# Performance work log

Hardware: AMD Instinct MI355X
Metric: run time of the kernel (lower is better)

## Reference

```python
import jax, jax.numpy as jnp
import numpy as np

# --- architecture constants (match init_kwargs) ---
SLEN = 104
PTILE = 8
STEP = 2
N_BANDS = 2
MAX_DET = 2
N_SRC_PARAMS = 2
ENC_C = 20
ENC_HIDDEN = 256
# dim_out_all = 0.5*D*(D+1)*(4+2*n_source_params) + 1 + D  (probs over n_sources + per-count loc/flux mean+logvar)
DIM_OUT = int(0.5 * MAX_DET * (MAX_DET + 1) * (4 + 2 * N_SRC_PARAMS)) + 1 + MAX_DET  # 27


def _p(key, shape, scale=0.02):
    return scale * jax.random.normal(key, shape, dtype=jnp.float32)


def setup_inputs() -> dict:
    key = jax.random.key(0)
    ks = jax.random.split(key, 14)
    flat_in = ENC_C * PTILE * PTILE  # 20*8*8 = 1280
    return {
        "images": jax.random.normal(ks[0], (32, N_BANDS, SLEN, SLEN), dtype=jnp.float32),
        "conv1_w": _p(ks[1], (ENC_C, N_BANDS, 3, 3)),
        "conv1_b": _p(ks[2], (ENC_C,)),
        "conv2_w": _p(ks[3], (ENC_C, ENC_C, 3, 3)),
        "conv2_b": _p(ks[4], (ENC_C,)),
        "fc1_w": _p(ks[5], (ENC_HIDDEN, flat_in)),
        "fc1_b": _p(ks[6], (ENC_HIDDEN,)),
        "fc2_w": _p(ks[7], (ENC_HIDDEN, ENC_HIDDEN)),
        "fc2_b": _p(ks[8], (ENC_HIDDEN,)),
        "fc3_w": _p(ks[9], (ENC_HIDDEN, ENC_HIDDEN)),
        "fc3_b": _p(ks[10], (ENC_HIDDEN,)),
        "fcf_w": _p(ks[11], (DIM_OUT, ENC_HIDDEN)),
        "fcf_b": _p(ks[12], (DIM_OUT,)),
    }


def _tile_images(images):
    # torch tile_images: (B, C, slen, slen) -> (B * n_ptiles, C, P, P), tiles row-major over (x, y)
    B, C = images.shape[0], images.shape[1]
    patches = jax.lax.conv_general_dilated_patches(
        images, filter_shape=(PTILE, PTILE), window_strides=(STEP, STEP), padding="VALID"
    )  # (B, C*P*P, Hn, Wn) with feature dim ordered (C, P, P)
    Hn, Wn = patches.shape[2], patches.shape[3]
    p = patches.reshape(B, C, PTILE, PTILE, Hn, Wn)
    p = p.transpose(0, 4, 5, 1, 2, 3)  # (B, Hn, Wn, C, P, P)
    return p.reshape(B * Hn * Wn, C, PTILE, PTILE)


def _conv(x, w, b):
    y = jax.lax.conv_general_dilated(
        x, w, window_strides=(1, 1), padding="SAME",
        dimension_numbers=("NCHW", "OIHW", "NCHW"),
    )
    return y + b[None, :, None, None]


def reference(images, conv1_w, conv1_b, conv2_w, conv2_b,
              fc1_w, fc1_b, fc2_w, fc2_b, fc3_w, fc3_b, fcf_w, fcf_b):
    ptiles = _tile_images(images)                       # (B*nT, C, P, P)
    h = jax.nn.relu(_conv(ptiles, conv1_w, conv1_b))    # (B*nT, 20, P, P)
    h = jax.nn.relu(_conv(h, conv2_w, conv2_b))
    h = h.reshape(h.shape[0], -1)                       # Flatten -> (B*nT, 1280)
    h = jax.nn.relu(h @ fc1_w.T + fc1_b)
    h = jax.nn.relu(h @ fc2_w.T + fc2_b)
    h = jax.nn.relu(h @ fc3_w.T + fc3_b)
    return h @ fcf_w.T + fcf_b                          # (B*nT, dim_out_all)
```

## Files before the change

kernel.cpp:

```cpp
#include <hip/hip_runtime.h>
#include <hip/hip_bf16.h>

#define NPATCH 76832
#define NBLK   601
#define K1     1280

typedef __attribute__((ext_vector_type(8))) short  short8;
typedef __attribute__((ext_vector_type(4))) float  floatx4;

__device__ __forceinline__ unsigned short f2b(float f) {
    unsigned int u = __builtin_bit_cast(unsigned int, f);
    u += 0x7FFFu + ((u >> 16) & 1u);
    return (unsigned short)(u >> 16);
}
__device__ __forceinline__ unsigned int pk2(float a, float b) {
    __hip_bfloat162 h = __float22bfloat162_rn(make_float2(a, b));
    unsigned int u;
    __builtin_memcpy(&u, &h, 4);
    return u;
}

__device__ __forceinline__ void gload_lds16(const unsigned short* g, unsigned short* l) {
    __builtin_amdgcn_global_load_lds(
        (__attribute__((address_space(1))) void*)g,
        (__attribute__((address_space(3))) void*)l,
        16, 0, 0);
}

__device__ __host__ __forceinline__ int swz8(int row, int i) {
    return (((row & 1) * 4 + i) ^ ((row >> 1) & 7));
}

__global__ void prep(const float* __restrict__ f1w, const float* __restrict__ f2w,
                     const float* __restrict__ f3w, const float* __restrict__ c1w,
                     const float* __restrict__ c2w, const float* __restrict__ ffw,
                     unsigned short* __restrict__ W1F, unsigned short* __restrict__ W2F,
                     unsigned short* __restrict__ W3F, unsigned short* __restrict__ W1T,
                     unsigned short* __restrict__ W2T, unsigned short* __restrict__ WfF) {
    int i = blockIdx.x * 256 + threadIdx.x;
    if (i < 327680) {
        int o = i / 1280, k = i - o * 1280;
        int dst = ((k >> 5) * 16 + (o >> 6) * 4 + ((o >> 4) & 3)) * 512
                + (((k >> 3) & 3) * 16 + (o & 15)) * 8 + (k & 7);
        W1F[dst] = f2b(f1w[i]);
        return;
    }
    i -= 327680;
    if (i < 65536) {
        int o = i >> 8, k = i & 255;
        int dst = ((k >> 5) * 16 + (o >> 6) * 4 + ((o >> 4) & 3)) * 512
                + (((k >> 3) & 3) * 16 + (o & 15)) * 8 + (k & 7);
        W2F[dst] = f2b(f2w[i]);
        return;
    }
    i -= 65536;
    if (i < 65536) {
        int o = i >> 8, k = i & 255;
        int dst = ((k >> 5) * 16 + (o >> 6) * 4 + ((o >> 4) & 3)) * 512
                + (((k >> 3) & 3) * 16 + (o & 15)) * 8 + (k & 7);
        W3F[dst] = f2b(f3w[i]);
        return;
    }
    i -= 65536;
    if (i < 1024) {
        int o = i >> 5, k = i & 31;
        unsigned short v = 0;
        if (o < 20 && k < 18) v = f2b(c1w[o * 18 + k]);
        W1T[(o >> 1) * 64 + swz8(o, k >> 3) * 8 + (k & 7)] = v;
        return;
    }
    i -= 1024;
    if (i < 9216) {
        int tap = i >> 10, rem = i & 1023, o = rem >> 5, c = rem & 31;
        unsigned short v = 0;
        if (o < 20 && c < 20) v = f2b(c2w[o * 180 + c * 9 + tap]);
        W2T[tap * 1024 + (o >> 1) * 64 + swz8(o, c >> 3) * 8 + (c & 7)] = v;
        return;
    }
    i -= 9216;
    if (i < 8192) {
        int o = i >> 8, k = i & 255;
        unsigned short v = (o < 27) ? f2b(ffw[o * 256 + k]) : (unsigned short)0;
        int dst = ((k >> 5) * 2 + (o >> 4)) * 512
                + (((k >> 3) & 3) * 16 + (o & 15)) * 8 + (k & 7);
        WfF[dst] = v;
    }
}

__global__ __launch_bounds__(256, 3) void conv_mfma(
    const float* __restrict__ img,
    const unsigned short* __restrict__ W1T, const float* __restrict__ b1,
    const unsigned short* __restrict__ W2T, const float* __restrict__ b2,
    unsigned short* __restrict__ X, int row0)
{
    __shared__ alignas(16) unsigned short s_buf[8 * 2048 + 64];
    __shared__ alignas(16) unsigned short s_w1t[1024];
    __shared__ alignas(16) unsigned short s_w2t[9216];
    __shared__ float s_b1[32], s_b2[32];
    constexpr int ZOFF = 8 * 2048;

    const int tid = threadIdx.x;
    for (int d = tid; d < 512; d += 256)  ((unsigned int*)s_w1t)[d] = ((const unsigned int*)W1T)[d];
    for (int d = tid; d < 4608; d += 256) ((unsigned int*)s_w2t)[d] = ((const unsigned int*)W2T)[d];
    if (tid < 32) {
        ((unsigned int*)&s_buf[ZOFF])[tid] = 0u;
        s_b1[tid] = (tid < 20) ? b1[tid] : 0.f;
        s_b2[tid] = (tid < 20) ? b2[tid] : 0.f;
    }

    const int q = tid >> 5, t = tid & 31;
    const int Pl = blockIdx.x * 8 + q;
    const int Pi = row0 + Pl;
    const bool valid = Pi < NPATCH;
    int b = 0, hi = 0, wi = 0;
    if (valid) { b = Pi / 2401; int rem = Pi - b * 2401; hi = rem / 49; wi = rem - hi * 49; }
    const int py = t >> 2, px0 = (t & 3) * 2;
    const float* ib = img + (long long)b * 21632 + (hi * 2) * 104 + (wi * 2);

    float win[2][3][4];
    #pragma unroll
    for (int c = 0; c < 2; ++c)
        #pragma unroll
        for (int dy = 0; dy < 3; ++dy) {
            int ny = py + dy - 1;
            int nyc = ny < 0 ? 0 : (ny > 7 ? 7 : ny);
            #pragma unroll
            for (int dxw = 0; dxw < 4; ++dxw) {
                int nx = px0 + dxw - 1;
                int nxc = nx < 0 ? 0 : (nx > 7 ? 7 : nx);
                win[c][dy][dxw] = ib[c * 10816 + nyc * 104 + nxc];
            }
        }

    #pragma unroll
    for (int j = 0; j < 2; ++j) {
        const int px = px0 + j, pl = py * 8 + px;
        float val[18];
        #pragma unroll
        for (int c = 0; c < 2; ++c)
            #pragma unroll
            for (int dy = 0; dy < 3; ++dy) {
                int ny = py + dy - 1;
                bool rok = valid && ((unsigned)ny < 8u);
                #pragma unroll
                for (int dx = 0; dx < 3; ++dx) {
                    int nx = px + dx - 1;
                    bool ok = rok && ((unsigned)nx < 8u);
                    val[c * 9 + dy * 3 + dx] = ok ? win[c][dy][dx + j] : 0.f;
                }
            }
        alignas(16) unsigned int au[16];
        #pragma unroll
        for (int i = 0; i < 9; ++i) au[i] = pk2(val[2 * i], val[2 * i + 1]);
        #pragma unroll
        for (int i = 9; i < 16; ++i) au[i] = 0u;
        unsigned short* base = &s_buf[q * 2048 + (pl >> 1) * 64];
        #pragma unroll
        for (int i = 0; i < 4; ++i)
            *(uint4*)&base[swz8(pl, i) * 8] = ((const uint4*)au)[i];
    }
    __syncthreads();

    const int wave = tid >> 6, lane = tid & 63;
    const int l15 = lane & 15, quad = lane >> 4;
    const int p0 = wave * 2;

    int boffB[2];
    #pragma unroll
    for (int i = 0; i < 2; ++i) {
        int oo = i * 16 + l15;
        boffB[i] = (oo >> 1) * 64 + swz8(oo, quad) * 8;
    }

    short8 a1f[2];
    #pragma unroll
    for (int mt = 0; mt < 2; ++mt) a1f[mt] = *(const short8*)&s_w1t[boffB[mt]];

    floatx4 acc1[2][2][4] = {};
    #pragma unroll
    for (int pp = 0; pp < 2; ++pp)
        #pragma unroll
        for (int nt = 0; nt < 4; ++nt) {
            int pix = nt * 16 + l15;
            short8 pf = *(const short8*)&s_buf[(p0 + pp) * 2048 + (pix >> 1) * 64 + swz8(pix, quad) * 8];
            #pragma unroll
            for (int mt = 0; mt < 2; ++mt)
                acc1[pp][mt][nt] = __builtin_amdgcn_mfma_f32_16x16x32_bf16(a1f[mt], pf, acc1[pp][mt][nt], 0, 0, 0);
        }

    float bv1[2][4];
    #pragma unroll
    for (int mt = 0; mt < 2; ++mt)
        #pragma unroll
        for (int r = 0; r < 4; ++r) bv1[mt][r] = s_b1[mt * 16 + quad * 4 + r];

    #pragma unroll
    for (int pp = 0; pp < 2; ++pp)
        #pragma unroll
        for (int mt = 0; mt < 2; ++mt)
            #pragma unroll
            for (int nt = 0; nt < 4; ++nt) {
                floatx4 v = acc1[pp][mt][nt];
                uint2 w;
                w.x = pk2(fmaxf(v[0] + bv1[mt][0], 0.f), fmaxf(v[1] + bv1[mt][1], 0.f));
                w.y = pk2(fmaxf(v[2] + bv1[mt][2], 0.f), fmaxf(v[3] + bv1[mt][3], 0.f));
                int pix = nt * 16 + l15;
                int off = (p0 + pp) * 2048 + (pix >> 1) * 64
                        + swz8(pix, mt * 2 + (quad >> 1)) * 8 + (quad & 1) * 4;
                *(uint2*)&s_buf[off] = w;
            }

    int syv[4], pxv[4];
    #pragma unroll
    for (int mt = 0; mt < 4; ++mt) { int p = mt * 16 + l15; syv[mt] = p >> 3; pxv[mt] = p & 7; }

    floatx4 acc2[2][4][2] = {};
    #pragma unroll 1
    for (int dy = 0; dy < 3; ++dy) {
        int sy[4]; bool okY[4];
        #pragma unroll
        for (int mt = 0; mt < 4; ++mt) {
            sy[mt] = syv[mt] + dy - 1;
            okY[mt] = (unsigned)sy[mt] < 8u;
        }
        #pragma unroll
        for (int dx = 0; dx < 3; ++dx) {
            const int tap = dy * 3 + dx;
            short8 bf0 = *(const short8*)&s_w2t[tap * 1024 + boffB[0]];
            short8 bf1 = *(const short8*)&s_w2t[tap * 1024 + boffB[1]];
            #pragma unroll
            for (int mt = 0; mt < 4; ++mt) {
                int sx = pxv[mt] + dx - 1;
                bool ok = okY[mt] & ((unsigned)sx < 8u);
                int ps = sy[mt] * 8 + sx;
                int offl = (ps >> 1) * 64 + swz8(ps, quad) * 8;
                #pragma unroll
                for (int pp = 0; pp < 2; ++pp) {
                    int off = ok ? ((p0 + pp) * 2048 + offl) : (ZOFF + quad * 8);
                    short8 af = *(const short8*)&s_buf[off];
                    acc2[pp][mt][0] = __builtin_amdgcn_mfma_f32_16x16x32_bf16(af, bf0, acc2[pp][mt][0], 0, 0, 0);
                    acc2[pp][mt][1] = __builtin_amdgcn_mfma_f32_16x16x32_bf16(af, bf1, acc2[pp][mt][1], 0, 0, 0);
                }
            }
        }
    }

    #pragma unroll
    for (int pp = 0; pp < 2; ++pp) {
        unsigned short* xrow = X + (long long)(blockIdx.x * 8 + p0 + pp) * K1;
        #pragma unroll
        for (int nt = 0; nt < 2; ++nt) {
            const int col = nt * 16 + l15;
            if (col < 20) {
                const float bv = s_b2[col];
                #pragma unroll
                for (int mt = 0; mt < 4; ++mt) {
                    floatx4 v = acc2[pp][mt][nt];
                    uint2 w;
                    w.x = pk2(fmaxf(v[0] + bv, 0.f), fmaxf(v[1] + bv, 0.f));
                    w.y = pk2(fmaxf(v[2] + bv, 0.f), fmaxf(v[3] + bv, 0.f));
                    *(uint2*)&xrow[col * 64 + mt * 16 + quad * 4] = w;
                }
            }
        }
    }
}

__global__ __launch_bounds__(256, 3) void fc_all(
    const unsigned short* __restrict__ X,
    const unsigned short* __restrict__ W1F, const unsigned short* __restrict__ W2F,
    const unsigned short* __restrict__ W3F, const unsigned short* __restrict__ WfF,
    const float* __restrict__ b1, const float* __restrict__ b2,
    const float* __restrict__ b3, const float* __restrict__ bf_,
    float* __restrict__ out, int row0)
{
    __shared__ alignas(16) unsigned short s_mem[16384];

    const int tid = threadIdx.x;
    const int m0 = blockIdx.x * 64;
    const int wave = tid >> 6, lane = tid & 63;
    const int l15 = lane & 15, quad = lane >> 4;

    floatx4 acc[4][4];
    #pragma unroll
    for (int mt = 0; mt < 4; ++mt)
        #pragma unroll
        for (int nt = 0; nt < 4; ++nt) acc[mt][nt] = floatx4{0.f, 0.f, 0.f, 0.f};

    const unsigned short* xsrc = X + (long long)(m0 + wave * 16 + l15) * 1280 + quad * 8;
    auto stage = [&](int buf, int c) {
        unsigned short* dst = &s_mem[buf * 4096 + wave * 512];
        gload_lds16(xsrc + (2 * c) * 32, dst);
        gload_lds16(xsrc + (2 * c + 1) * 32, dst + 2048);
    };

    stage(0, 0);
    __syncthreads();
    #pragma unroll 2
    for (int c = 0; c < 20; ++c) {
        short8 af[2][4];
        #pragma unroll
        for (int kh = 0; kh < 2; ++kh)
            #pragma unroll
            for (int mt = 0; mt < 4; ++mt)
                af[kh][mt] = *(const short8*)(W1F + (((2 * c + kh) * 16) + wave * 4 + mt) * 512 + lane * 8);
        __builtin_amdgcn_sched_barrier(0);
        if (c < 19) stage((c + 1) & 1, c + 1);
        const int bb = (c & 1) * 4096;
        __builtin_amdgcn_s_setprio(1);
        #pragma unroll
        for (int kh = 0; kh < 2; ++kh) {
            short8 bf[4];
            #pragma unroll
            for (int nt = 0; nt < 4; ++nt)
                bf[nt] = *(const short8*)&s_mem[bb + (kh * 4 + nt) * 512 + lane * 8];
            #pragma unroll
            for (int mt = 0; mt < 4; ++mt)
                #pragma unroll
                for (int nt = 0; nt < 4; ++nt)
                    acc[mt][nt] = __builtin_amdgcn_mfma_f32_16x16x32_bf16(af[kh][mt], bf[nt], acc[mt][nt], 0, 0, 0);
        }
        __builtin_amdgcn_s_setprio(0);
        __syncthreads();
    }

    #pragma unroll
    for (int mt = 0; mt < 4; ++mt) {
        const int obase = wave * 64 + mt * 16 + quad * 4;
        const float v0 = b1[obase], v1 = b1[obase + 1], v2 = b1[obase + 2], v3 = b1[obase + 3];
        const int slot = (wave * 2 + (mt >> 1)) * 4;
        const int qk = (mt & 1) * 2 + (quad >> 1);
        #pragma unroll
        for (int nt = 0; nt < 4; ++nt) {
            floatx4 v = acc[mt][nt];
            uint2 w;
            w.x = pk2(fmaxf(v[0] + v0, 0.f), fmaxf(v[1] + v1, 0.f));
            w.y = pk2(fmaxf(v[2] + v2, 0.f), fmaxf(v[3] + v3, 0.f));
            *(uint2*)&s_mem[(slot + nt) * 512 + qk * 128 + l15 * 8 + (quad & 1) * 4] = w;
        }
    }
    __syncthreads();

    #pragma unroll 1
    for (int layer = 0; layer < 2; ++layer) {
        const unsigned short* Wp = (layer == 0) ? W2F : W3F;
        const float* bp = (layer == 0) ? b2 : b3;

        #pragma unroll
        for (int mt = 0; mt < 4; ++mt)
            #pragma unroll
            for (int nt = 0; nt < 4; ++nt) acc[mt][nt] = floatx4{0.f, 0.f, 0.f, 0.f};

        short8 afc[4];
        #pragma unroll
        for (int mt = 0; mt < 4; ++mt)
            afc[mt] = *(const short8*)(Wp + (wave * 4 + mt) * 512 + lane * 8);

        #pragma unroll
        for (int it = 0; it < 8; ++it) {
            short8 afn[4];
            if (it < 7) {
                #pragma unroll
                for (int mt = 0; mt < 4; ++mt)
                    afn[mt] = *(const short8*)(Wp + ((it + 1) * 16 + wave * 4 + mt) * 512 + lane * 8);
            }
            short8 bf[4];
            #pragma unroll
            for (int nt = 0; nt < 4; ++nt)
                bf[nt] = *(const short8*)&s_mem[(it * 4 + nt) * 512 + lane * 8];
            __builtin_amdgcn_s_setprio(1);
            #pragma unroll
            for (int mt = 0; mt < 4; ++mt)
                #pragma unroll
                for (int nt = 0; nt < 4; ++nt)
                    acc[mt][nt] = __builtin_amdgcn_mfma_f32_16x16x32_bf16(afc[mt], bf[nt], acc[mt][nt], 0, 0, 0);
            __builtin_amdgcn_s_setprio(0);
            if (it < 7) {
                #pragma unroll
                for (int mt = 0; mt < 4; ++mt) afc[mt] = afn[mt];
            }
        }
        __syncthreads();
        #pragma unroll
        for (int mt = 0; mt < 4; ++mt) {
            const int obase = wave * 64 + mt * 16 + quad * 4;
            const float v0 = bp[obase], v1 = bp[obase + 1], v2 = bp[obase + 2], v3 = bp[obase + 3];
            const int slot = (wave * 2 + (mt >> 1)) * 4;
            const int qk = (mt & 1) * 2 + (quad >> 1);
            #pragma unroll
            for (int nt = 0; nt < 4; ++nt) {
                floatx4 v = acc[mt][nt];
                uint2 w;
                w.x = pk2(fmaxf(v[0] + v0, 0.f), fmaxf(v[1] + v1, 0.f));
                w.y = pk2(fmaxf(v[2] + v2, 0.f), fmaxf(v[3] + v3, 0.f));
                *(uint2*)&s_mem[(slot + nt) * 512 + qk * 128 + l15 * 8 + (quad & 1) * 4] = w;
            }
        }
        __syncthreads();
    }

    floatx4 accf[2] = {floatx4{0.f, 0.f, 0.f, 0.f}, floatx4{0.f, 0.f, 0.f, 0.f}};
    const int myrow = wave * 16 + l15;
    #pragma unroll
    for (int w8 = 0; w8 < 8; ++w8) {
        short8 bfr = *(const short8*)&s_mem[(w8 * 4 + wave) * 512 + lane * 8];
        #pragma unroll
        for (int mt = 0; mt < 2; ++mt) {
            short8 afr = *(const short8*)(WfF + (w8 * 2 + mt) * 512 + lane * 8);
            accf[mt] = __builtin_amdgcn_mfma_f32_16x16x32_bf16(afr, bfr, accf[mt], 0, 0, 0);
        }
    }
    const int grow = row0 + m0 + myrow;
    if (grow < NPATCH) {
        #pragma unroll
        for (int mt = 0; mt < 2; ++mt) {
            #pragma unroll
            for (int r = 0; r < 4; ++r) {
                int o = mt * 16 + quad * 4 + r;
                if (o < 27)
                    out[(long long)grow * 27 + o] = accf[mt][r] + bf_[o];
            }
        }
    }
}

extern "C" void kernel_launch(void* const* d_in, const int* in_sizes, int n_in,
                              void* d_out, int out_size, void* d_ws, size_t ws_size,
                              hipStream_t stream) {
    const float* images = (const float*)d_in[0];
    const float* c1w = (const float*)d_in[1];
    const float* c1b = (const float*)d_in[2];
    const float* c2w = (const float*)d_in[3];
    const float* c2b = (const float*)d_in[4];
    const float* f1w = (const float*)d_in[5];
    const float* f1b = (const float*)d_in[6];
    const float* f2w = (const float*)d_in[7];
    const float* f2b_ = (const float*)d_in[8];
    const float* f3w = (const float*)d_in[9];
    const float* f3b = (const float*)d_in[10];
    const float* ffw = (const float*)d_in[11];
    const float* ffb = (const float*)d_in[12];

    const long long W1_E = 327680, W2_E = 65536, W3_E = 65536;
    const long long W1T_E = 1024, W2T_E = 9216, WF_E = 8192;
    const long long WB = (W1_E + W2_E + W3_E + W1T_E + W2T_E + WF_E) * 2;
    char* ws = (char*)d_ws;
    unsigned short* W1F = (unsigned short*)ws;
    unsigned short* W2F = W1F + W1_E;
    unsigned short* W3F = W2F + W2_E;
    unsigned short* W1T = W3F + W3_E;
    unsigned short* W2T = W1T + W1T_E;
    unsigned short* WfF = W2T + W2T_E;
    unsigned short* X   = (unsigned short*)(ws + WB);

    long long avail = (long long)ws_size - WB - 256;
    int nb_max = (int)(avail / 327680LL);
    if (nb_max < 1) nb_max = 1;
    if (nb_max > NBLK) nb_max = NBLK;
    int nchunks = (NBLK + nb_max - 1) / nb_max;
    int nb_even = (NBLK + nchunks - 1) / nchunks;

    prep<<<1864, 256, 0, stream>>>(f1w, f2w, f3w, c1w, c2w, ffw, W1F, W2F, W3F, W1T, W2T, WfF);

    for (int b0 = 0; b0 < NBLK; b0 += nb_even) {
        int nb = NBLK - b0; if (nb > nb_even) nb = nb_even;
        int row0 = b0 * 128;
        int rows = nb * 128;

        conv_mfma<<<rows / 8, 256, 0, stream>>>(images, W1T, c1b, W2T, c2b, X, row0);
        fc_all<<<rows / 64, 256, 0, stream>>>(X, W1F, W2F, W3F, WfF,
                                              f1b, f2b_, f3b, ffb, (float*)d_out, row0);
    }
}
```

Measured before the change: 293.5 us.

## Drop LDS weight staging in conv kernel and prefetch fc1 weights in registers

The conv kernel no longer copies the conv weights and biases into shared memory. Each wave loads its weight fragments and biases straight from global memory, and the block-wide barrier after patch staging is removed because each wave only reads patches its own lanes wrote. Zero padding now reads a known-zero slot inside the patch buffer instead of a separate zero region. Smaller LDS use and launch_bounds raised to 4 are meant to raise occupancy. fc_all double-buffers the fc1 weight fragments in registers so the next chunk's weights load while the current chunk's MFMAs run, at the cost of more VGPRs.

After: 605.7 us. 2.06x slower.

```diff
diff --git a/kernel.cpp b/kernel.cpp
--- a/kernel.cpp
+++ b/kernel.cpp
@@ -87,25 +87,43 @@
     }
 }
 
-__global__ __launch_bounds__(256, 3) void conv_mfma(
+__global__ __launch_bounds__(256, 4) void conv_mfma(
     const float* __restrict__ img,
     const unsigned short* __restrict__ W1T, const float* __restrict__ b1,
     const unsigned short* __restrict__ W2T, const float* __restrict__ b2,
     unsigned short* __restrict__ X, int row0)
 {
-    __shared__ alignas(16) unsigned short s_buf[8 * 2048 + 64];
-    __shared__ alignas(16) unsigned short s_w1t[1024];
-    __shared__ alignas(16) unsigned short s_w2t[9216];
-    __shared__ float s_b1[32], s_b2[32];
-    constexpr int ZOFF = 8 * 2048;
+    __shared__ alignas(16) unsigned short s_buf[8 * 2048];
 
     const int tid = threadIdx.x;
-    for (int d = tid; d < 512; d += 256)  ((unsigned int*)s_w1t)[d] = ((const unsigned int*)W1T)[d];
-    for (int d = tid; d < 4608; d += 256) ((unsigned int*)s_w2t)[d] = ((const unsigned int*)W2T)[d];
-    if (tid < 32) {
-        ((unsigned int*)&s_buf[ZOFF])[tid] = 0u;
-        s_b1[tid] = (tid < 20) ? b1[tid] : 0.f;
-        s_b2[tid] = (tid < 20) ? b2[tid] : 0.f;
+    const int wave = tid >> 6, lane = tid & 63;
+    const int l15 = lane & 15, quad = lane >> 4;
+
+    int boffB[2];
+    #pragma unroll
+    for (int i = 0; i < 2; ++i) {
+        int oo = i * 16 + l15;
+        boffB[i] = (oo >> 1) * 64 + swz8(oo, quad) * 8;
+    }
+
+    short8 a1f[2];
+    #pragma unroll
+    for (int mt = 0; mt < 2; ++mt) a1f[mt] = *(const short8*)(W1T + boffB[mt]);
+    float bv1[2][4];
+    #pragma unroll
+    for (int mt = 0; mt < 2; ++mt)
+        #pragma unroll
+        for (int r = 0; r < 4; ++r) {
+            int idx = mt * 16 + quad * 4 + r;
+            float v = b1[idx < 20 ? idx : 19];
+            bv1[mt][r] = (idx < 20) ? v : 0.f;
+        }
+    float bv2[2];
+    #pragma unroll
+    for (int nt = 0; nt < 2; ++nt) {
+        int col = nt * 16 + l15;
+        float v = b2[col < 20 ? col : 19];
+        bv2[nt] = (col < 20) ? v : 0.f;
     }
 
     const int q = tid >> 5, t = tid & 31;
@@ -159,22 +177,8 @@
         for (int i = 0; i < 4; ++i)
             *(uint4*)&base[swz8(pl, i) * 8] = ((const uint4*)au)[i];
     }
-    __syncthreads();
-
-    const int wave = tid >> 6, lane = tid & 63;
-    const int l15 = lane & 15, quad = lane >> 4;
+
     const int p0 = wave * 2;
-
-    int boffB[2];
-    #pragma unroll
-    for (int i = 0; i < 2; ++i) {
-        int oo = i * 16 + l15;
-        boffB[i] = (oo >> 1) * 64 + swz8(oo, quad) * 8;
-    }
-
-    short8 a1f[2];
-    #pragma unroll
-    for (int mt = 0; mt < 2; ++mt) a1f[mt] = *(const short8*)&s_w1t[boffB[mt]];
 
     floatx4 acc1[2][2][4] = {};
     #pragma unroll
@@ -187,12 +191,6 @@
             for (int mt = 0; mt < 2; ++mt)
                 acc1[pp][mt][nt] = __builtin_amdgcn_mfma_f32_16x16x32_bf16(a1f[mt], pf, acc1[pp][mt][nt], 0, 0, 0);
         }
-
-    float bv1[2][4];
-    #pragma unroll
-    for (int mt = 0; mt < 2; ++mt)
-        #pragma unroll
-        for (int r = 0; r < 4; ++r) bv1[mt][r] = s_b1[mt * 16 + quad * 4 + r];
 
     #pragma unroll
     for (int pp = 0; pp < 2; ++pp)
@@ -226,18 +224,18 @@
         #pragma unroll
         for (int dx = 0; dx < 3; ++dx) {
             const int tap = dy * 3 + dx;
-            short8 bf0 = *(const short8*)&s_w2t[tap * 1024 + boffB[0]];
-            short8 bf1 = *(const short8*)&s_w2t[tap * 1024 + boffB[1]];
+            short8 bf0 = *(const short8*)(W2T + tap * 1024 + boffB[0]);
+            short8 bf1 = *(const short8*)(W2T + tap * 1024 + boffB[1]);
             #pragma unroll
             for (int mt = 0; mt < 4; ++mt) {
                 int sx = pxv[mt] + dx - 1;
                 bool ok = okY[mt] & ((unsigned)sx < 8u);
                 int ps = sy[mt] * 8 + sx;
                 int offl = (ps >> 1) * 64 + swz8(ps, quad) * 8;
+                int offz = ok ? offl : 24;
                 #pragma unroll
                 for (int pp = 0; pp < 2; ++pp) {
-                    int off = ok ? ((p0 + pp) * 2048 + offl) : (ZOFF + quad * 8);
-                    short8 af = *(const short8*)&s_buf[off];
+                    short8 af = *(const short8*)&s_buf[(p0 + pp) * 2048 + offz];
                     acc2[pp][mt][0] = __builtin_amdgcn_mfma_f32_16x16x32_bf16(af, bf0, acc2[pp][mt][0], 0, 0, 0);
                     acc2[pp][mt][1] = __builtin_amdgcn_mfma_f32_16x16x32_bf16(af, bf1, acc2[pp][mt][1], 0, 0, 0);
                 }
@@ -252,7 +250,7 @@
         for (int nt = 0; nt < 2; ++nt) {
             const int col = nt * 16 + l15;
             if (col < 20) {
-                const float bv = s_b2[col];
+                const float bv = bv2[nt];
                 #pragma unroll
                 for (int mt = 0; mt < 4; ++mt) {
                     floatx4 v = acc2[pp][mt][nt];
@@ -293,20 +291,29 @@
         gload_lds16(xsrc + (2 * c) * 32, dst);
         gload_lds16(xsrc + (2 * c + 1) * 32, dst + 2048);
     };
-
+    const unsigned short* wsrc = W1F + (wave * 4) * 512 + lane * 8;
+
+    short8 af[2][2][4];
+    #pragma unroll
+    for (int kh = 0; kh < 2; ++kh)
+        #pragma unroll
+        for (int mt = 0; mt < 4; ++mt)
+            af[0][kh][mt] = *(const short8*)(wsrc + (kh * 16 + mt) * 512);
     stage(0, 0);
     __syncthreads();
     #pragma unroll 2
     for (int c = 0; c < 20; ++c) {
-        short8 af[2][4];
-        #pragma unroll
-        for (int kh = 0; kh < 2; ++kh)
-            #pragma unroll
-            for (int mt = 0; mt < 4; ++mt)
-                af[kh][mt] = *(const short8*)(W1F + (((2 * c + kh) * 16) + wave * 4 + mt) * 512 + lane * 8);
+        const int pb = c & 1;
+        if (c < 19) {
+            #pragma unroll
+            for (int kh = 0; kh < 2; ++kh)
+                #pragma unroll
+                for (int mt = 0; mt < 4; ++mt)
+                    af[pb ^ 1][kh][mt] = *(const short8*)(wsrc + (((2 * (c + 1) + kh) * 16 + mt)) * 512);
+        }
         __builtin_amdgcn_sched_barrier(0);
         if (c < 19) stage((c + 1) & 1, c + 1);
-        const int bb = (c & 1) * 4096;
+        const int bb = pb * 4096;
         __builtin_amdgcn_s_setprio(1);
         #pragma unroll
         for (int kh = 0; kh < 2; ++kh) {
@@ -318,7 +325,7 @@
             for (int mt = 0; mt < 4; ++mt)
                 #pragma unroll
                 for (int nt = 0; nt < 4; ++nt)
-                    acc[mt][nt] = __builtin_amdgcn_mfma_f32_16x16x32_bf16(af[kh][mt], bf[nt], acc[mt][nt], 0, 0, 0);
+                    acc[mt][nt] = __builtin_amdgcn_mfma_f32_16x16x32_bf16(af[pb][kh][mt], bf[nt], acc[mt][nt], 0, 0, 0);
         }
         __builtin_amdgcn_s_setprio(0);
         __syncthreads();
```
